# Kernel tuning notes

Hardware: AMD Instinct MI355X
Metric: run time of the kernel (lower is better)

## Reference

```python
import jax, jax.numpy as jnp
import numpy as np

D_MODEL = 1024
N_HEADS = 16
D_K = D_MODEL // N_HEADS


def setup_inputs() -> dict:
    key = jax.random.key(0)
    ks = jax.random.split(key, 12)
    B, S = 4, 2048
    scale = 1.0 / np.sqrt(D_MODEL)
    inp = {
        "Q_in": jax.random.normal(ks[0], (B, S, D_MODEL), jnp.float32),
        "K_in": jax.random.normal(ks[1], (B, S, D_MODEL), jnp.float32),
        "V_in": jax.random.normal(ks[2], (B, S, D_MODEL), jnp.float32),
        "Wq": jax.random.normal(ks[3], (D_MODEL, D_MODEL), jnp.float32) * scale,
        "bq": jnp.zeros((D_MODEL,), jnp.float32),
        "Wk": jax.random.normal(ks[4], (D_MODEL, D_MODEL), jnp.float32) * scale,
        "bk": jnp.zeros((D_MODEL,), jnp.float32),
        "Wv": jax.random.normal(ks[5], (D_MODEL, D_MODEL), jnp.float32) * scale,
        "bv": jnp.zeros((D_MODEL,), jnp.float32),
        "Wo": jax.random.normal(ks[6], (D_MODEL, D_MODEL), jnp.float32) * scale,
        "bo": jnp.zeros((D_MODEL,), jnp.float32),
    }
    return inp


def reference(Q_in, K_in, V_in, Wq, bq, Wk, bk, Wv, bv, Wo, bo):
    B, S, _ = Q_in.shape
    # QKV projections, split into heads: [B, H, S, d_k]
    def proj(x, W, b):
        y = jnp.einsum('bsd,df->bsf', x, W) + b
        return y.reshape(B, S, N_HEADS, D_K).transpose(0, 2, 1, 3)

    Q = proj(Q_in, Wq, bq)
    K = proj(K_in, Wk, bk)
    V = proj(V_in, Wv, bv)

    # scaled dot-product attention (dropout is identity in eval)
    scores = jnp.einsum('bhqd,bhkd->bhqk', Q, K) / jnp.sqrt(jnp.float32(D_K)).astype(Q.dtype)
    p_attn = jax.nn.softmax(scores, axis=-1)
    x = jnp.einsum('bhqk,bhkd->bhqd', p_attn, V)

    # merge heads and output projection
    x = x.transpose(0, 2, 1, 3).reshape(B, S, D_MODEL)
    return jnp.einsum('bsd,df->bsf', x, Wo) + bo
```

## Files before the change

### kernel.cpp

```cpp
#include <hip/hip_runtime.h>

#define DEV __device__ __forceinline__

typedef _Float16 f16;
typedef __attribute__((ext_vector_type(8))) _Float16 f16x8;
typedef __attribute__((ext_vector_type(4))) _Float16 f16x4;
typedef __attribute__((ext_vector_type(2))) __fp16 fp16v2;
typedef __attribute__((ext_vector_type(4))) float floatx4;

constexpr int DMODEL = 1024;
constexpr int SLEN = 2048;
constexpr float SCALE_Q = 0.125f * 1.4426950408889634f;

DEV void gll16(const void* g, void* lds) {
    __builtin_amdgcn_global_load_lds((const __attribute__((address_space(1))) void*)g,
                                     (__attribute__((address_space(3))) void*)lds, 16, 0, 0);
}

#if __has_builtin(__builtin_amdgcn_exp2f)
DEV float fast_exp2(float x) { return __builtin_amdgcn_exp2f(x); }
#else
DEV float fast_exp2(float x) { return __expf(x * 0.6931471805599453f); }
#endif

DEV unsigned pkh2(float a, float b) {
    union { fp16v2 h; unsigned u; } c;
    c.h = __builtin_amdgcn_cvt_pkrtz(a, b);
    return c.u;
}

#if __has_builtin(__builtin_amdgcn_permlane32_swap) && __has_builtin(__builtin_amdgcn_permlane16_swap)
DEV void pl32swap(unsigned& x, unsigned& y) {
    auto r = __builtin_amdgcn_permlane32_swap(x, y, false, false);
    x = r[0]; y = r[1];
}
DEV void pl16swap(unsigned& x, unsigned& y) {
    auto r = __builtin_amdgcn_permlane16_swap(x, y, false, false);
    x = r[0]; y = r[1];
}
#else
DEV void pl32swap(unsigned& x, unsigned& y) {
    unsigned xs = (unsigned)__shfl_xor((int)x, 32, 64);
    unsigned ys = (unsigned)__shfl_xor((int)y, 32, 64);
    bool lo = (threadIdx.x & 63) < 32;
    unsigned nx = lo ? x : ys, ny = lo ? xs : y;
    x = nx; y = ny;
}
DEV void pl16swap(unsigned& x, unsigned& y) {
    unsigned xs = (unsigned)__shfl_xor((int)x, 16, 64);
    unsigned ys = (unsigned)__shfl_xor((int)y, 16, 64);
    bool ev = (((threadIdx.x & 63) >> 4) & 1) == 0;
    unsigned nx = ev ? x : ys, ny = ev ? xs : y;
    x = nx; y = ny;
}
#endif

DEV f16x8 xform(const floatx4& s0, const floatx4& s1) {
    unsigned X  = pkh2(fast_exp2(s0[0]), fast_exp2(s0[1]));
    unsigned Xp = pkh2(fast_exp2(s0[2]), fast_exp2(s0[3]));
    unsigned Y  = pkh2(fast_exp2(s1[0]), fast_exp2(s1[1]));
    unsigned Yp = pkh2(fast_exp2(s1[2]), fast_exp2(s1[3]));
    pl32swap(X, Y);  pl16swap(X, Y);
    pl32swap(Xp, Yp); pl16swap(Xp, Yp);
    union { unsigned u[4]; f16x8 v; } o;
    o.u[0] = X; o.u[1] = Xp; o.u[2] = Y; o.u[3] = Yp;
    return o.v;
}

__global__ void cvt3(const float* __restrict__ A0, const float* __restrict__ A1,
                     const float* __restrict__ A2, f16* __restrict__ O0,
                     f16* __restrict__ O1, f16* __restrict__ O2) {
    const int seg = blockIdx.x >> 12;
    const int i = (blockIdx.x & 4095) * 256 + threadIdx.x;
    const float* in = seg == 0 ? A0 : seg == 1 ? A1 : A2;
    f16* out = seg == 0 ? O0 : seg == 1 ? O1 : O2;
    const float4 a = ((const float4*)in)[2 * i];
    const float4 b = ((const float4*)in)[2 * i + 1];
    f16x8 h;
    h[0] = (f16)a.x; h[1] = (f16)a.y; h[2] = (f16)a.z; h[3] = (f16)a.w;
    h[4] = (f16)b.x; h[5] = (f16)b.y; h[6] = (f16)b.z; h[7] = (f16)b.w;
    ((f16x8*)out)[i] = h;
}

__global__ void wtrans4(const float* __restrict__ W0, const float* __restrict__ W1,
                        const float* __restrict__ W2, const float* __restrict__ W3,
                        f16* __restrict__ T0, f16* __restrict__ T1,
                        f16* __restrict__ T2, f16* __restrict__ T3) {
    __shared__ float t[32][33];
    const int w = blockIdx.x >> 10, bid = blockIdx.x & 1023;
    const float* W = w == 0 ? W0 : w == 1 ? W1 : w == 2 ? W2 : W3;
    f16* Wt = w == 0 ? T0 : w == 1 ? T1 : w == 2 ? T2 : T3;
    const int tn = bid & 31, tk = bid >> 5;
    const int c = threadIdx.x & 31, r0 = threadIdx.x >> 5;
    for (int i = 0; i < 4; ++i) {
        int r = r0 + i * 8;
        t[r][c] = W[(tk * 32 + r) * DMODEL + tn * 32 + c];
    }
    __syncthreads();
    for (int i = 0; i < 4; ++i) {
        int r = r0 + i * 8;
        Wt[(tn * 32 + r) * DMODEL + tk * 32 + c] = (f16)t[c][r];
    }
}

DEV void gemm_core(const f16* __restrict__ A, const f16* __restrict__ Bt,
                   f16* smem, int row0, int col0, int tid, floatx4 (&acc)[4][4]) {
    const int wid = tid >> 6, lane = tid & 63;
    const int quad = lane >> 4, l16 = lane & 15;
    const int wm = (wid >> 1) * 64, wn = (wid & 1) * 64;
    const int off = wid * 1024 + lane * 16;
    const int r = off >> 6, cb = (off & 63) >> 1;

    {
        gll16(Bt + (col0 + r) * DMODEL + cb, (char*)(smem + 4096) + wid * 1024);
        gll16(Bt + (col0 + r + 64) * DMODEL + cb, (char*)(smem + 4096) + 4096 + wid * 1024);
        gll16(A + (row0 + r) * DMODEL + cb, (char*)smem + wid * 1024);
        gll16(A + (row0 + r + 64) * DMODEL + cb, (char*)smem + 4096 + wid * 1024);
    }
    for (int it = 0; it < 32; ++it) {
        f16* As = smem + (it & 1) * 8192;
        f16* Bs = As + 4096;
        if (it < 31) {
            const int k0 = (it + 1) * 32;
            f16* An = smem + ((it + 1) & 1) * 8192;
            f16* Bn = An + 4096;
            gll16(Bt + (col0 + r) * DMODEL + k0 + cb, (char*)Bn + wid * 1024);
            gll16(Bt + (col0 + r + 64) * DMODEL + k0 + cb, (char*)Bn + 4096 + wid * 1024);
            gll16(A + (row0 + r) * DMODEL + k0 + cb, (char*)An + wid * 1024);
            gll16(A + (row0 + r + 64) * DMODEL + k0 + cb, (char*)An + 4096 + wid * 1024);
            __builtin_amdgcn_s_waitcnt(0xF74);
        } else {
            __builtin_amdgcn_s_waitcnt(0xF70);
        }
        __builtin_amdgcn_s_barrier();

        f16x8 af[4], bf[4];
        for (int mi = 0; mi < 4; ++mi)
            af[mi] = *(const f16x8*)&As[(wm + mi * 16 + l16) * 32 + quad * 8];
        for (int ni = 0; ni < 4; ++ni)
            bf[ni] = *(const f16x8*)&Bs[(wn + ni * 16 + l16) * 32 + quad * 8];
        for (int mi = 0; mi < 4; ++mi)
            for (int ni = 0; ni < 4; ++ni)
                acc[mi][ni] = __builtin_amdgcn_mfma_f32_16x16x32_f16(af[mi], bf[ni], acc[mi][ni], 0, 0, 0);
        __builtin_amdgcn_s_barrier();
    }
}

__global__ __launch_bounds__(256, 3)
void gemm_qkv(const f16* __restrict__ A0, const f16* __restrict__ A1, const f16* __restrict__ A2,
              const f16* __restrict__ B0, const f16* __restrict__ B1, const f16* __restrict__ B2,
              const float* __restrict__ bi0, const float* __restrict__ bi1, const float* __restrict__ bi2,
              f16* __restrict__ C0, f16* __restrict__ C1, f16* __restrict__ C2, int epi_base) {
    __shared__ f16 smem[16384];
    const int seg = blockIdx.x >> 9, inner = blockIdx.x & 511;
    const int epi = epi_base + seg;
    const f16* A = seg == 0 ? A0 : seg == 1 ? A1 : A2;
    const f16* Bt = seg == 0 ? B0 : seg == 1 ? B1 : B2;
    const float* bias = seg == 0 ? bi0 : seg == 1 ? bi1 : bi2;
    f16* Cp = seg == 0 ? C0 : seg == 1 ? C1 : C2;

    const int tid = threadIdx.x;
    const int wid = tid >> 6, lane = tid & 63;
    const int quad = lane >> 4, l16 = lane & 15;
    const int bm = inner & 63, bn = inner >> 6;
    const int row0 = bm * 128, col0 = bn * 128;
    const int wm = (wid >> 1) * 64, wn = (wid & 1) * 64;

    floatx4 acc[4][4];
    for (int i = 0; i < 4; ++i)
        for (int j = 0; j < 4; ++j) acc[i][j] = {0.f, 0.f, 0.f, 0.f};

    gemm_core(A, Bt, smem, row0, col0, tid, acc);

    const float scale = (epi == 0) ? SCALE_Q : 1.0f;
    for (int mi = 0; mi < 4; ++mi) {
        for (int ni = 0; ni < 4; ++ni) {
            const int gr0 = row0 + wm + mi * 16 + quad * 4;
            const int gc = col0 + wn + ni * 16 + l16;
            const float bv = bias[gc];
            if (epi == 2) {
                const int b_ = gr0 >> 11, s0 = gr0 & 2047;
                const int h_ = gc >> 6, d_ = gc & 63;
                const int bh = b_ * 16 + h_;
                const int csw = ((s0 >> 3) & 15) ^ (d_ & 7);
                const int s0w = (s0 & ~127) | (csw << 3) | (s0 & 7);
                f16x4 o;
                for (int r = 0; r < 4; ++r) o[r] = (f16)(acc[mi][ni][r] + bv);
                *(f16x4*)&Cp[(bh * 64 + d_) * SLEN + s0w] = o;
            } else {
                for (int r = 0; r < 4; ++r) {
                    const int gr = gr0 + r;
                    const int b_ = gr >> 11, s_ = gr & 2047;
                    const int h_ = gc >> 6, d_ = gc & 63;
                    const int bh = b_ * 16 + h_;
                    const int dsw = (((d_ >> 3) ^ (s_ & 7)) << 3) | (d_ & 7);
                    Cp[(bh * SLEN + s_) * 64 + dsw] = (f16)((acc[mi][ni][r] + bv) * scale);
                }
            }
        }
    }
}

__global__ __launch_bounds__(256, 3)
void gemm_out(const f16* __restrict__ A, const f16* __restrict__ Bt,
              const float* __restrict__ bias, float* __restrict__ Cp) {
    __shared__ f16 smem[16384];
    const int tid = threadIdx.x;
    const int wid = tid >> 6, lane = tid & 63;
    const int quad = lane >> 4, l16 = lane & 15;
    const int bm = blockIdx.x & 63, bn = blockIdx.x >> 6;
    const int row0 = bm * 128, col0 = bn * 128;
    const int wm = (wid >> 1) * 64, wn = (wid & 1) * 64;

    floatx4 acc[4][4];
    for (int i = 0; i < 4; ++i)
        for (int j = 0; j < 4; ++j) acc[i][j] = {0.f, 0.f, 0.f, 0.f};

    gemm_core(A, Bt, smem, row0, col0, tid, acc);

    for (int mi = 0; mi < 4; ++mi)
        for (int ni = 0; ni < 4; ++ni) {
            const int gr0 = row0 + wm + mi * 16 + quad * 4;
            const int gc = col0 + wn + ni * 16 + l16;
            const float bv = bias[gc];
            for (int r = 0; r < 4; ++r)
                Cp[(gr0 + r) * DMODEL + gc] = acc[mi][ni][r] + bv;
        }
}

__global__ __launch_bounds__(256, 2)
void flash_k(const f16* __restrict__ Qh, const f16* __restrict__ Kh,
             const f16* __restrict__ Vt, f16* __restrict__ attn) {
    __shared__ f16 smem[32768];
    const int tid = threadIdx.x;
    const int wid = tid >> 6, lane = tid & 63;
    const int quad = lane >> 4, l16 = lane & 15;
    const int xcd = blockIdx.x & 7, jj = blockIdx.x >> 3;
    const int bh = xcd * 8 + (jj & 7), qt = jj >> 3;
    const int wq = wid * 64;

    f16* Qs = smem + 16384;
    const f16* Qbase = Qh + (bh * SLEN + qt * 256) * 64;
#pragma unroll
    for (int j = 0; j < 8; ++j) {
        const int ch = j * 4 + wid;
        gll16(Qbase + ch * 512 + lane * 8, (char*)Qs + ch * 1024);
    }
    __syncthreads();

    f16x8 qf[4][2];
#pragma unroll
    for (int nq = 0; nq < 4; ++nq)
#pragma unroll
        for (int kc = 0; kc < 2; ++kc)
            qf[nq][kc] = *(const f16x8*)&Qs[(wq + nq * 16 + l16) * 64 +
                                            (((kc * 4 + quad) ^ (l16 & 7)) << 3)];
    __syncthreads();

    floatx4 oacc[4][5];
    for (int nq = 0; nq < 4; ++nq)
        for (int md = 0; md < 5; ++md) oacc[nq][md] = {0.f, 0.f, 0.f, 0.f};

    const f16x8 ones = {(f16)1, (f16)1, (f16)1, (f16)1, (f16)1, (f16)1, (f16)1, (f16)1};
    const f16* Kb = Kh + bh * SLEN * 64;
    const f16* Vb = Vt + bh * 64 * SLEN;

#pragma unroll
    for (int j = 0; j < 4; ++j) {
        const int ch = j * 4 + wid;
        gll16(Kb + ch * 512 + lane * 8, (char*)smem + ch * 1024);
        const int ci = ch * 64 + lane;
        gll16(Vb + (ci >> 4) * SLEN + (ci & 15) * 8, (char*)(smem + 8192) + ch * 1024);
    }

    for (int t = 0; t < 16; ++t) {
        f16* Ks = smem + (t & 1) * 16384;
        f16* Vs = Ks + 8192;
        if (t < 15) {
            const int kv0n = (t + 1) * 128;
            f16* Kn = smem + ((t + 1) & 1) * 16384;
            f16* Vn = Kn + 8192;
#pragma unroll
            for (int j = 0; j < 4; ++j) {
                const int ch = j * 4 + wid;
                gll16(Kb + kv0n * 64 + ch * 512 + lane * 8, (char*)Kn + ch * 1024);
                const int ci = ch * 64 + lane;
                gll16(Vb + (ci >> 4) * SLEN + kv0n + (ci & 15) * 8, (char*)Vn + ch * 1024);
            }
            __builtin_amdgcn_s_waitcnt(0xF78);
        } else {
            __builtin_amdgcn_s_waitcnt(0xF70);
        }
        __builtin_amdgcn_s_barrier();

        f16x8 pf[4];
#pragma unroll
        for (int c = 0; c < 4; ++c) {
            floatx4 sacc[4][2];
            for (int nq = 0; nq < 4; ++nq)
                for (int t2 = 0; t2 < 2; ++t2) sacc[nq][t2] = {0.f, 0.f, 0.f, 0.f};
#pragma unroll
            for (int t2 = 0; t2 < 2; ++t2) {
                const int a = c * 2 + t2;
#pragma unroll
                for (int kc = 0; kc < 2; ++kc) {
                    f16x8 kf = *(const f16x8*)&Ks[(a * 16 + l16) * 64 +
                                                  (((kc * 4 + quad) ^ (l16 & 7)) << 3)];
                    for (int nq = 0; nq < 4; ++nq)
                        sacc[nq][t2] = __builtin_amdgcn_mfma_f32_16x16x32_f16(
                            kf, qf[nq][kc], sacc[nq][t2], 0, 0, 0);
                }
            }
            if (c > 0) {
                const int cp = c - 1;
#pragma unroll
                for (int md = 0; md < 4; ++md) {
                    f16x8 vf = *(const f16x8*)&Vs[(md * 16 + l16) * 128 +
                                                  (((cp * 4 + quad) ^ (l16 & 7)) << 3)];
                    for (int nq = 0; nq < 4; ++nq)
                        oacc[nq][md] = __builtin_amdgcn_mfma_f32_16x16x32_f16(
                            vf, pf[nq], oacc[nq][md], 0, 0, 0);
                }
                for (int nq = 0; nq < 4; ++nq)
                    oacc[nq][4] = __builtin_amdgcn_mfma_f32_16x16x32_f16(
                        ones, pf[nq], oacc[nq][4], 0, 0, 0);
            }
#pragma unroll
            for (int nq = 0; nq < 4; ++nq) pf[nq] = xform(sacc[nq][0], sacc[nq][1]);
        }
#pragma unroll
        for (int md = 0; md < 4; ++md) {
            f16x8 vf = *(const f16x8*)&Vs[(md * 16 + l16) * 128 +
                                          (((3 * 4 + quad) ^ (l16 & 7)) << 3)];
            for (int nq = 0; nq < 4; ++nq)
                oacc[nq][md] = __builtin_amdgcn_mfma_f32_16x16x32_f16(
                    vf, pf[nq], oacc[nq][md], 0, 0, 0);
        }
        for (int nq = 0; nq < 4; ++nq)
            oacc[nq][4] = __builtin_amdgcn_mfma_f32_16x16x32_f16(
                ones, pf[nq], oacc[nq][4], 0, 0, 0);

        __builtin_amdgcn_s_barrier();
    }

    const int b_ = bh >> 4, h_ = bh & 15;
#pragma unroll
    for (int nq = 0; nq < 4; ++nq) {
        const float linv = __frcp_rn(oacc[nq][4][0]);
        const int tok = b_ * SLEN + qt * 256 + wq + nq * 16 + l16;
#pragma unroll
        for (int md = 0; md < 4; ++md) {
            f16x4 o;
            for (int r = 0; r < 4; ++r) o[r] = (f16)(oacc[nq][md][r] * linv);
            *(f16x4*)&attn[tok * DMODEL + h_ * 64 + md * 16 + quad * 4] = o;
        }
    }
}

extern "C" void kernel_launch(void* const* d_in, const int* in_sizes, int n_in,
                              void* d_out, int out_size, void* d_ws, size_t ws_size,
                              hipStream_t stream) {
    (void)in_sizes; (void)n_in; (void)out_size;
    const float* Q_in = (const float*)d_in[0];
    const float* K_in = (const float*)d_in[1];
    const float* V_in = (const float*)d_in[2];
    const float* Wq = (const float*)d_in[3];
    const float* bq = (const float*)d_in[4];
    const float* Wk = (const float*)d_in[5];
    const float* bk = (const float*)d_in[6];
    const float* Wv = (const float*)d_in[7];
    const float* bv = (const float*)d_in[8];
    const float* Wo = (const float*)d_in[9];
    const float* bo = (const float*)d_in[10];
    float* out = (float*)d_out;

    char* ws = (char*)d_ws;
    const size_t MB = 1u << 20;
    f16* wtq = (f16*)(ws + 0 * MB);
    f16* wtk = (f16*)(ws + 2 * MB);
    f16* wtv = (f16*)(ws + 4 * MB);
    f16* wto = (f16*)(ws + 6 * MB);
    f16* Qh  = (f16*)(ws + 8 * MB);
    f16* Kh  = (f16*)(ws + 24 * MB);
    f16* Vt  = (f16*)(ws + 40 * MB);
    f16* At  = (f16*)(ws + 56 * MB);

    wtrans4<<<4096, 256, 0, stream>>>(Wq, Wk, Wv, Wo, wtq, wtk, wtv, wto);

    if (ws_size >= 120 * MB) {
        f16* Ac0 = (f16*)(ws + 72 * MB);
        f16* Ac1 = (f16*)(ws + 88 * MB);
        f16* Ac2 = (f16*)(ws + 104 * MB);
        cvt3<<<3 * 4096, 256, 0, stream>>>(Q_in, K_in, V_in, Ac0, Ac1, Ac2);
        gemm_qkv<<<1536, 256, 0, stream>>>(Ac0, Ac1, Ac2, wtq, wtk, wtv,
                                           bq, bk, bv, Qh, Kh, Vt, 0);
    } else {
        f16* Ac = At;
        cvt3<<<4096, 256, 0, stream>>>(Q_in, Q_in, Q_in, Ac, Ac, Ac);
        gemm_qkv<<<512, 256, 0, stream>>>(Ac, Ac, Ac, wtq, wtq, wtq, bq, bq, bq,
                                          Qh, Qh, Qh, 0);
        cvt3<<<4096, 256, 0, stream>>>(K_in, K_in, K_in, Ac, Ac, Ac);
        gemm_qkv<<<512, 256, 0, stream>>>(Ac, Ac, Ac, wtk, wtk, wtk, bk, bk, bk,
                                          Kh, Kh, Kh, 1);
        cvt3<<<4096, 256, 0, stream>>>(V_in, V_in, V_in, Ac, Ac, Ac);
        gemm_qkv<<<512, 256, 0, stream>>>(Ac, Ac, Ac, wtv, wtv, wtv, bv, bv, bv,
                                          Vt, Vt, Vt, 2);
    }

    flash_k<<<512, 256, 0, stream>>>(Qh, Kh, Vt, At);
    gemm_out<<<512, 256, 0, stream>>>(At, wto, bo, out);
}
```

Before: 323.7 us.

## Fuse fp32-to-fp16 input conversion into QKV GEMM A-tile loading

Removes the separate cvt3 kernel and has gemm_qkv read the fp32 activations directly into registers, convert them to fp16 and store them into LDS, prefetching the next K-slice while B still uses global_load_lds. This drops a full fp32 read and fp16 write/read round-trip of the three 32 MB inputs and one kernel launch. In exchange, A loads go through VGPRs with a custom waitcnt and a sched barrier, which may raise register pressure or expose latency. The flash kernel also initializes each score accumulation from a zero constant instead of explicitly zeroing sacc.

```diff
diff --git a/kernel.cpp b/kernel.cpp
--- a/kernel.cpp
+++ b/kernel.cpp
@@ -16,6 +16,14 @@
     __builtin_amdgcn_global_load_lds((const __attribute__((address_space(1))) void*)g,
                                      (__attribute__((address_space(3))) void*)lds, 16, 0, 0);
 }
+
+#if __has_builtin(__builtin_amdgcn_sched_barrier)
+#define SCHED_FENCE() __builtin_amdgcn_sched_barrier(0)
+constexpr int WAIT_BDRAIN = 0x076;
+#else
+#define SCHED_FENCE()
+constexpr int WAIT_BDRAIN = 0x072;
+#endif
 
 #if __has_builtin(__builtin_amdgcn_exp2f)
 DEV float fast_exp2(float x) { return __builtin_amdgcn_exp2f(x); }
@@ -65,21 +73,6 @@
     union { unsigned u[4]; f16x8 v; } o;
     o.u[0] = X; o.u[1] = Xp; o.u[2] = Y; o.u[3] = Yp;
     return o.v;
-}
-
-__global__ void cvt3(const float* __restrict__ A0, const float* __restrict__ A1,
-                     const float* __restrict__ A2, f16* __restrict__ O0,
-                     f16* __restrict__ O1, f16* __restrict__ O2) {
-    const int seg = blockIdx.x >> 12;
-    const int i = (blockIdx.x & 4095) * 256 + threadIdx.x;
-    const float* in = seg == 0 ? A0 : seg == 1 ? A1 : A2;
-    f16* out = seg == 0 ? O0 : seg == 1 ? O1 : O2;
-    const float4 a = ((const float4*)in)[2 * i];
-    const float4 b = ((const float4*)in)[2 * i + 1];
-    f16x8 h;
-    h[0] = (f16)a.x; h[1] = (f16)a.y; h[2] = (f16)a.z; h[3] = (f16)a.w;
-    h[4] = (f16)b.x; h[5] = (f16)b.y; h[6] = (f16)b.z; h[7] = (f16)b.w;
-    ((f16x8*)out)[i] = h;
 }
 
 __global__ void wtrans4(const float* __restrict__ W0, const float* __restrict__ W1,
@@ -103,34 +96,68 @@
     }
 }
 
-DEV void gemm_core(const f16* __restrict__ A, const f16* __restrict__ Bt,
+template <bool A32>
+DEV void gemm_core(const void* __restrict__ Ap, const f16* __restrict__ Bt,
                    f16* smem, int row0, int col0, int tid, floatx4 (&acc)[4][4]) {
     const int wid = tid >> 6, lane = tid & 63;
     const int quad = lane >> 4, l16 = lane & 15;
     const int wm = (wid >> 1) * 64, wn = (wid & 1) * 64;
     const int off = wid * 1024 + lane * 16;
     const int r = off >> 6, cb = (off & 63) >> 1;
-
-    {
-        gll16(Bt + (col0 + r) * DMODEL + cb, (char*)(smem + 4096) + wid * 1024);
-        gll16(Bt + (col0 + r + 64) * DMODEL + cb, (char*)(smem + 4096) + 4096 + wid * 1024);
-        gll16(A + (row0 + r) * DMODEL + cb, (char*)smem + wid * 1024);
-        gll16(A + (row0 + r + 64) * DMODEL + cb, (char*)smem + 4096 + wid * 1024);
-    }
+    const int arow = tid >> 3, acol = (tid & 7) * 4;
+
+    const float* A32p = (const float*)Ap;
+    const f16* A16p = (const f16*)Ap;
+    float4 Aregs[4];
+
+    if constexpr (A32) {
+#pragma unroll
+        for (int p = 0; p < 4; ++p)
+            Aregs[p] = *(const float4*)&A32p[(row0 + arow + p * 32) * DMODEL + acol];
+    } else {
+        gll16(A16p + (row0 + r) * DMODEL + cb, (char*)smem + wid * 1024);
+        gll16(A16p + (row0 + r + 64) * DMODEL + cb, (char*)smem + 4096 + wid * 1024);
+    }
+    gll16(Bt + (col0 + r) * DMODEL + cb, (char*)(smem + 4096) + wid * 1024);
+    gll16(Bt + (col0 + r + 64) * DMODEL + cb, (char*)(smem + 4096) + 4096 + wid * 1024);
+
     for (int it = 0; it < 32; ++it) {
         f16* As = smem + (it & 1) * 8192;
         f16* Bs = As + 4096;
-        if (it < 31) {
-            const int k0 = (it + 1) * 32;
-            f16* An = smem + ((it + 1) & 1) * 8192;
-            f16* Bn = An + 4096;
-            gll16(Bt + (col0 + r) * DMODEL + k0 + cb, (char*)Bn + wid * 1024);
-            gll16(Bt + (col0 + r + 64) * DMODEL + k0 + cb, (char*)Bn + 4096 + wid * 1024);
-            gll16(A + (row0 + r) * DMODEL + k0 + cb, (char*)An + wid * 1024);
-            gll16(A + (row0 + r + 64) * DMODEL + k0 + cb, (char*)An + 4096 + wid * 1024);
-            __builtin_amdgcn_s_waitcnt(0xF74);
+        if constexpr (A32) {
+#pragma unroll
+            for (int p = 0; p < 4; ++p) {
+                unsigned u0 = pkh2(Aregs[p].x, Aregs[p].y);
+                unsigned u1 = pkh2(Aregs[p].z, Aregs[p].w);
+                uint2 uu; uu.x = u0; uu.y = u1;
+                *(uint2*)&As[(arow + p * 32) * 32 + acol] = uu;
+            }
+            if (it < 31) {
+                const int k0n = (it + 1) * 32;
+#pragma unroll
+                for (int p = 0; p < 4; ++p)
+                    Aregs[p] = *(const float4*)&A32p[(row0 + arow + p * 32) * DMODEL + k0n + acol];
+                f16* Bn = smem + ((it + 1) & 1) * 8192 + 4096;
+                gll16(Bt + (col0 + r) * DMODEL + k0n + cb, (char*)Bn + wid * 1024);
+                gll16(Bt + (col0 + r + 64) * DMODEL + k0n + cb, (char*)Bn + 4096 + wid * 1024);
+                SCHED_FENCE();
+                __builtin_amdgcn_s_waitcnt(WAIT_BDRAIN);
+            } else {
+                __builtin_amdgcn_s_waitcnt(0x070);
+            }
         } else {
-            __builtin_amdgcn_s_waitcnt(0xF70);
+            if (it < 31) {
+                const int k0n = (it + 1) * 32;
+                f16* An = smem + ((it + 1) & 1) * 8192;
+                f16* Bn = An + 4096;
+                gll16(Bt + (col0 + r) * DMODEL + k0n + cb, (char*)Bn + wid * 1024);
+                gll16(Bt + (col0 + r + 64) * DMODEL + k0n + cb, (char*)Bn + 4096 + wid * 1024);
+                gll16(A16p + (row0 + r) * DMODEL + k0n + cb, (char*)An + wid * 1024);
+                gll16(A16p + (row0 + r + 64) * DMODEL + k0n + cb, (char*)An + 4096 + wid * 1024);
+                __builtin_amdgcn_s_waitcnt(0xF74);
+            } else {
+                __builtin_amdgcn_s_waitcnt(0xF70);
+            }
         }
         __builtin_amdgcn_s_barrier();
 
@@ -147,14 +174,13 @@
 }
 
 __global__ __launch_bounds__(256, 3)
-void gemm_qkv(const f16* __restrict__ A0, const f16* __restrict__ A1, const f16* __restrict__ A2,
+void gemm_qkv(const float* __restrict__ A0, const float* __restrict__ A1, const float* __restrict__ A2,
               const f16* __restrict__ B0, const f16* __restrict__ B1, const f16* __restrict__ B2,
               const float* __restrict__ bi0, const float* __restrict__ bi1, const float* __restrict__ bi2,
-              f16* __restrict__ C0, f16* __restrict__ C1, f16* __restrict__ C2, int epi_base) {
+              f16* __restrict__ C0, f16* __restrict__ C1, f16* __restrict__ C2) {
     __shared__ f16 smem[16384];
     const int seg = blockIdx.x >> 9, inner = blockIdx.x & 511;
-    const int epi = epi_base + seg;
-    const f16* A = seg == 0 ? A0 : seg == 1 ? A1 : A2;
+    const float* A = seg == 0 ? A0 : seg == 1 ? A1 : A2;
     const f16* Bt = seg == 0 ? B0 : seg == 1 ? B1 : B2;
     const float* bias = seg == 0 ? bi0 : seg == 1 ? bi1 : bi2;
     f16* Cp = seg == 0 ? C0 : seg == 1 ? C1 : C2;
@@ -170,31 +196,31 @@
     for (int i = 0; i < 4; ++i)
         for (int j = 0; j < 4; ++j) acc[i][j] = {0.f, 0.f, 0.f, 0.f};
 
-    gemm_core(A, Bt, smem, row0, col0, tid, acc);
-
-    const float scale = (epi == 0) ? SCALE_Q : 1.0f;
+    gemm_core<true>(A, Bt, smem, row0, col0, tid, acc);
+
+    const float scale = (seg == 0) ? SCALE_Q : 1.0f;
     for (int mi = 0; mi < 4; ++mi) {
         for (int ni = 0; ni < 4; ++ni) {
             const int gr0 = row0 + wm + mi * 16 + quad * 4;
             const int gc = col0 + wn + ni * 16 + l16;
             const float bv = bias[gc];
-            if (epi == 2) {
+            if (seg == 2) {
                 const int b_ = gr0 >> 11, s0 = gr0 & 2047;
                 const int h_ = gc >> 6, d_ = gc & 63;
                 const int bh = b_ * 16 + h_;
                 const int csw = ((s0 >> 3) & 15) ^ (d_ & 7);
                 const int s0w = (s0 & ~127) | (csw << 3) | (s0 & 7);
                 f16x4 o;
-                for (int r = 0; r < 4; ++r) o[r] = (f16)(acc[mi][ni][r] + bv);
+                for (int rr = 0; rr < 4; ++rr) o[rr] = (f16)(acc[mi][ni][rr] + bv);
                 *(f16x4*)&Cp[(bh * 64 + d_) * SLEN + s0w] = o;
             } else {
-                for (int r = 0; r < 4; ++r) {
-                    const int gr = gr0 + r;
+                for (int rr = 0; rr < 4; ++rr) {
+                    const int gr = gr0 + rr;
                     const int b_ = gr >> 11, s_ = gr & 2047;
                     const int h_ = gc >> 6, d_ = gc & 63;
                     const int bh = b_ * 16 + h_;
                     const int dsw = (((d_ >> 3) ^ (s_ & 7)) << 3) | (d_ & 7);
-                    Cp[(bh * SLEN + s_) * 64 + dsw] = (f16)((acc[mi][ni][r] + bv) * scale);
+                    Cp[(bh * SLEN + s_) * 64 + dsw] = (f16)((acc[mi][ni][rr] + bv) * scale);
                 }
             }
         }
@@ -216,15 +242,15 @@
     for (int i = 0; i < 4; ++i)
         for (int j = 0; j < 4; ++j) acc[i][j] = {0.f, 0.f, 0.f, 0.f};
 
-    gemm_core(A, Bt, smem, row0, col0, tid, acc);
+    gemm_core<false>(A, Bt, smem, row0, col0, tid, acc);
 
     for (int mi = 0; mi < 4; ++mi)
         for (int ni = 0; ni < 4; ++ni) {
             const int gr0 = row0 + wm + mi * 16 + quad * 4;
             const int gc = col0 + wn + ni * 16 + l16;
             const float bv = bias[gc];
-            for (int r = 0; r < 4; ++r)
-                Cp[(gr0 + r) * DMODEL + gc] = acc[mi][ni][r] + bv;
+            for (int rr = 0; rr < 4; ++rr)
+                Cp[(gr0 + rr) * DMODEL + gc] = acc[mi][ni][rr] + bv;
         }
 }
 
@@ -260,6 +286,7 @@
     floatx4 oacc[4][5];
     for (int nq = 0; nq < 4; ++nq)
         for (int md = 0; md < 5; ++md) oacc[nq][md] = {0.f, 0.f, 0.f, 0.f};
+    const floatx4 fzero = {0.f, 0.f, 0.f, 0.f};
 
     const f16x8 ones = {(f16)1, (f16)1, (f16)1, (f16)1, (f16)1, (f16)1, (f16)1, (f16)1};
     const f16* Kb = Kh + bh * SLEN * 64;
@@ -297,19 +324,17 @@
 #pragma unroll
         for (int c = 0; c < 4; ++c) {
             floatx4 sacc[4][2];
-            for (int nq = 0; nq < 4; ++nq)
-                for (int t2 = 0; t2 < 2; ++t2) sacc[nq][t2] = {0.f, 0.f, 0.f, 0.f};
 #pragma unroll
             for (int t2 = 0; t2 < 2; ++t2) {
                 const int a = c * 2 + t2;
-#pragma unroll
-                for (int kc = 0; kc < 2; ++kc) {
-                    f16x8 kf = *(const f16x8*)&Ks[(a * 16 + l16) * 64 +
-                                                  (((kc * 4 + quad) ^ (l16 & 7)) << 3)];
-                    for (int nq = 0; nq < 4; ++nq)
-                        sacc[nq][t2] = __builtin_amdgcn_mfma_f32_16x16x32_f16(
-                            kf, qf[nq][kc], sacc[nq][t2], 0, 0, 0);
-                }
+                f16x8 kf0 = *(const f16x8*)&Ks[(a * 16 + l16) * 64 + ((quad ^ (l16 & 7)) << 3)];
+                for (int nq = 0; nq < 4; ++nq)
+                    sacc[nq][t2] = __builtin_amdgcn_mfma_f32_16x16x32_f16(
+                        kf0, qf[nq][0], fzero, 0, 0, 0);
+                f16x8 kf1 = *(const f16x8*)&Ks[(a * 16 + l16) * 64 + (((4 + quad) ^ (l16 & 7)) << 3)];
+                for (int nq = 0; nq < 4; ++nq)
+                    sacc[nq][t2] = __builtin_amdgcn_mfma_f32_16x16x32_f16(
+                        kf1, qf[nq][1], sacc[nq][t2], 0, 0, 0);
             }
             if (c > 0) {
                 const int cp = c - 1;
@@ -351,7 +376,7 @@
 #pragma unroll
         for (int md = 0; md < 4; ++md) {
             f16x4 o;
-            for (int r = 0; r < 4; ++r) o[r] = (f16)(oacc[nq][md][r] * linv);
+            for (int rr = 0; rr < 4; ++rr) o[rr] = (f16)(oacc[nq][md][rr] * linv);
             *(f16x4*)&attn[tok * DMODEL + h_ * 64 + md * 16 + quad * 4] = o;
         }
     }
@@ -360,7 +385,7 @@
 extern "C" void kernel_launch(void* const* d_in, const int* in_sizes, int n_in,
                               void* d_out, int out_size, void* d_ws, size_t ws_size,
                               hipStream_t stream) {
-    (void)in_sizes; (void)n_in; (void)out_size;
+    (void)in_sizes; (void)n_in; (void)out_size; (void)ws_size;
     const float* Q_in = (const float*)d_in[0];
     const float* K_in = (const float*)d_in[1];
     const float* V_in = (const float*)d_in[2];
@@ -386,27 +411,8 @@
     f16* At  = (f16*)(ws + 56 * MB);
 
     wtrans4<<<4096, 256, 0, stream>>>(Wq, Wk, Wv, Wo, wtq, wtk, wtv, wto);
-
-    if (ws_size >= 120 * MB) {
-        f16* Ac0 = (f16*)(ws + 72 * MB);
-        f16* Ac1 = (f16*)(ws + 88 * MB);
-        f16* Ac2 = (f16*)(ws + 104 * MB);
-        cvt3<<<3 * 4096, 256, 0, stream>>>(Q_in, K_in, V_in, Ac0, Ac1, Ac2);
-        gemm_qkv<<<1536, 256, 0, stream>>>(Ac0, Ac1, Ac2, wtq, wtk, wtv,
-                                           bq, bk, bv, Qh, Kh, Vt, 0);
-    } else {
-        f16* Ac = At;
-        cvt3<<<4096, 256, 0, stream>>>(Q_in, Q_in, Q_in, Ac, Ac, Ac);
-        gemm_qkv<<<512, 256, 0, stream>>>(Ac, Ac, Ac, wtq, wtq, wtq, bq, bq, bq,
-                                          Qh, Qh, Qh, 0);
-        cvt3<<<4096, 256, 0, stream>>>(K_in, K_in, K_in, Ac, Ac, Ac);
-        gemm_qkv<<<512, 256, 0, stream>>>(Ac, Ac, Ac, wtk, wtk, wtk, bk, bk, bk,
-                                          Kh, Kh, Kh, 1);
-        cvt3<<<4096, 256, 0, stream>>>(V_in, V_in, V_in, Ac, Ac, Ac);
-        gemm_qkv<<<512, 256, 0, stream>>>(Ac, Ac, Ac, wtv, wtv, wtv, bv, bv, bv,
-                                          Vt, Vt, Vt, 2);
-    }
-
+    gemm_qkv<<<1536, 256, 0, stream>>>(Q_in, K_in, V_in, wtq, wtk, wtv,
+                                       bq, bk, bv, Qh, Kh, Vt);
     flash_k<<<512, 256, 0, stream>>>(Qh, Kh, Vt, At);
     gemm_out<<<512, 256, 0, stream>>>(At, wto, bo, out);
 }
```

After: 332.3 us. 2.7% more time.
